# Performance work log

Hardware: AMD Instinct MI355X
Metric: run time of the kernel (lower is better)

Reference implementation:

```python
import jax, jax.numpy as jnp
import numpy as np

FEAT = 512
COND = 768
N_HEADS = 8
D_HEAD = 64
D_ATTN = N_HEADS * D_HEAD  # 512


def setup_inputs() -> dict:
    key = jax.random.key(0)
    ks = jax.random.split(key, 8)
    B, N, M = 16, 4096, 77
    x = jax.random.normal(ks[0], (B, N, FEAT), dtype=jnp.float32)
    cond = jax.random.normal(ks[1], (B, M, COND), dtype=jnp.float32)
    s_f = 1.0 / np.sqrt(FEAT)
    s_c = 1.0 / np.sqrt(COND)
    s_a = 1.0 / np.sqrt(D_ATTN)
    Wq = jax.random.normal(ks[2], (FEAT, D_ATTN), dtype=jnp.float32) * s_f
    Wk = jax.random.normal(ks[3], (COND, D_ATTN), dtype=jnp.float32) * s_c
    Wv = jax.random.normal(ks[4], (COND, D_ATTN), dtype=jnp.float32) * s_c
    Wo = jax.random.normal(ks[5], (D_ATTN, FEAT), dtype=jnp.float32) * s_a
    bo = jax.random.normal(ks[6], (FEAT,), dtype=jnp.float32) * 0.01
    return {"x": x, "cond": cond, "Wq": Wq, "Wk": Wk, "Wv": Wv, "Wo": Wo, "bo": bo}


def reference(x, cond, Wq, Wk, Wv, Wo, bo):
    B, N, _ = x.shape
    M = cond.shape[1]
    scale = D_HEAD ** (-0.5)
    # projections (no bias, as in nn.Linear(..., bias=False))
    q = (x @ Wq).reshape(B, N, N_HEADS, D_HEAD)
    k = (cond @ Wk).reshape(B, M, N_HEADS, D_HEAD)
    v = (cond @ Wv).reshape(B, M, N_HEADS, D_HEAD)
    attn = jnp.einsum('bihd,bjhd->bhij', q, k) * scale  # [B,H,N,M]
    attn = jax.nn.softmax(attn, axis=-1)  # split-half inplace softmax == plain softmax
    out = jnp.einsum('bhij,bjhd->bihd', attn, v).reshape(B, N, D_ATTN)
    return out @ Wo + bo
```

## Files before the change

### kernel.cpp

```cpp
#include <hip/hip_runtime.h>

typedef __attribute__((ext_vector_type(8))) _Float16 f16x8;
typedef __attribute__((ext_vector_type(4))) float f32x4;

#define B_SZ   16
#define N_SEQ  4096
#define M_CTX  77
#define M_PAD  96
#define NH     8

__device__ __forceinline__ _Float16 f2h(float x) { return (_Float16)x; }

__device__ __forceinline__ void gload16(const void* g, void* l) {
    __builtin_amdgcn_global_load_lds(
        (const __attribute__((address_space(1))) unsigned int*)g,
        (__attribute__((address_space(3))) unsigned int*)l, 16, 0, 0);
}

template<int C>
__device__ __forceinline__ float dppf(float x) {
    union { float f; int i; } u, v;
    u.f = x;
    v.i = __builtin_amdgcn_mov_dpp(u.i, C, 0xF, 0xF, true);
    return v.f;
}
__device__ __forceinline__ float rmax16(float x) {
    x = fmaxf(x, dppf<0xB1>(x));
    x = fmaxf(x, dppf<0x4E>(x));
    x = fmaxf(x, dppf<0x141>(x));
    x = fmaxf(x, dppf<0x140>(x));
    return x;
}
__device__ __forceinline__ float rsum16(float x) {
    x += dppf<0xB1>(x);
    x += dppf<0x4E>(x);
    x += dppf<0x141>(x);
    x += dppf<0x140>(x);
    return x;
}

__global__ __launch_bounds__(256)
void convert(const float4* __restrict__ x, f16x8* __restrict__ xh, int n8)
{
    int idx = blockIdx.x * 256 + threadIdx.x;
    int stride = gridDim.x * 256;
    for (int i = idx; i < n8; i += stride) {
        float4 a = x[2 * i];
        float4 b = x[2 * i + 1];
        f16x8 o;
        o[0] = f2h(a.x); o[1] = f2h(a.y); o[2] = f2h(a.z); o[3] = f2h(a.w);
        o[4] = f2h(b.x); o[5] = f2h(b.y); o[6] = f2h(b.z); o[7] = f2h(b.w);
        xh[i] = o;
    }
}

__global__ __launch_bounds__(256)
void prep(const float* __restrict__ Wq, const float* __restrict__ Wk,
          const float* __restrict__ Wv, const float* __restrict__ Wo,
          _Float16* __restrict__ WqT, _Float16* __restrict__ WkT,
          _Float16* __restrict__ WvT, _Float16* __restrict__ WoT)
{
    __shared__ float t[32][33];
    const float* W; _Float16* WT; int K; float scale = 1.0f;
    switch (blockIdx.z) {
        case 0:  W = Wq; WT = WqT; K = 512; scale = 0.125f; break;
        case 1:  W = Wk; WT = WkT; K = 768; break;
        case 2:  W = Wv; WT = WvT; K = 768; break;
        default: W = Wo; WT = WoT; K = 512; break;
    }
    const int ky = blockIdx.y;
    if (ky * 32 >= K) return;
    const int nx = blockIdx.x;
    const int tr = threadIdx.x >> 5, tc = threadIdx.x & 31;
#pragma unroll
    for (int i = 0; i < 4; ++i) {
        int kr = tr + i * 8;
        t[kr][tc] = W[(size_t)(ky * 32 + kr) * 512 + nx * 32 + tc];
    }
    __syncthreads();
#pragma unroll
    for (int i = 0; i < 4; ++i) {
        int nr = tr + i * 8;
        WT[(size_t)(nx * 32 + nr) * K + ky * 32 + tc] = f2h(t[tc][nr] * scale);
    }
}

__global__ __launch_bounds__(256)
void kv_proj(const float* __restrict__ cond, const _Float16* __restrict__ WkT,
             const _Float16* __restrict__ WvT, _Float16* __restrict__ Kswz,
             _Float16* __restrict__ Vswz)
{
    const int tid = threadIdx.x;
    const int l = tid & 63, w = tid >> 6;
    const int lrow = l & 15, lk = l >> 4;
    const int h = blockIdx.x, b = blockIdx.y, which = blockIdx.z;
    const _Float16* WT = which ? WvT : WkT;
    const float* cb = cond + (size_t)b * M_CTX * 768;

    f32x4 acc[5];
#pragma unroll
    for (int i = 0; i < 5; ++i)
#pragma unroll
        for (int e = 0; e < 4; ++e) acc[i][e] = 0.f;

    const int n = h * 64 + w * 16 + lrow;
    for (int kk = 0; kk < 24; ++kk) {
        f16x8 bfrag = *(const f16x8*)(WT + (size_t)n * 768 + kk * 32 + lk * 8);
#pragma unroll
        for (int rt = 0; rt < 5; ++rt) {
            int m = rt * 16 + lrow;
            f16x8 afrag;
#pragma unroll
            for (int j = 0; j < 8; ++j) afrag[j] = (_Float16)0.f;
            if (m < M_CTX) {
                const float* a = cb + (size_t)m * 768 + kk * 32 + lk * 8;
                float4 f0 = *(const float4*)a;
                float4 f1 = *(const float4*)(a + 4);
                afrag[0] = f2h(f0.x); afrag[1] = f2h(f0.y);
                afrag[2] = f2h(f0.z); afrag[3] = f2h(f0.w);
                afrag[4] = f2h(f1.x); afrag[5] = f2h(f1.y);
                afrag[6] = f2h(f1.z); afrag[7] = f2h(f1.w);
            }
            acc[rt] = __builtin_amdgcn_mfma_f32_16x16x32_f16(afrag, bfrag, acc[rt], 0, 0, 0);
        }
    }

    const int bh = b * NH + h;
    const int d = w * 16 + lrow;
    const int dhi = d >> 3, dlo = d & 7;
    if (which == 0) {
        _Float16* Kb = Kswz + (size_t)bh * (M_PAD * 64);
#pragma unroll
        for (int rt = 0; rt < 5; ++rt)
#pragma unroll
            for (int r = 0; r < 4; ++r) {
                int m = rt * 16 + lk * 4 + r;
                Kb[m * 64 + ((dhi ^ (m & 7)) * 8) + dlo] = f2h(acc[rt][r]);
            }
#pragma unroll
        for (int r = 0; r < 4; ++r) {
            int m = 80 + lk * 4 + r;
            Kb[m * 64 + ((dhi ^ (m & 7)) * 8) + dlo] = (_Float16)0.f;
        }
    } else {
        _Float16* Vb = Vswz + (size_t)bh * (64 * 128);
#pragma unroll
        for (int rt = 0; rt < 5; ++rt)
#pragma unroll
            for (int r = 0; r < 4; ++r) {
                int m = rt * 16 + lk * 4 + r;
                Vb[d * 128 + (((m >> 3) ^ dlo) * 8) + (m & 7)] = f2h(acc[rt][r]);
            }
#pragma unroll
        for (int r = 0; r < 4; ++r) {
            int m = 80 + lk * 4 + r;
            Vb[d * 128 + (((m >> 3) ^ dlo) * 8) + (m & 7)] = (_Float16)0.f;
        }
    }
}

template<int EMODE>
__global__ __launch_bounds__(256)
void gemm512(const _Float16* __restrict__ A, const _Float16* __restrict__ BT,
             void* __restrict__ Cv, const float* __restrict__ bias)
{
    __shared__ _Float16 As[128 * 64];
    __shared__ _Float16 Bs[128 * 64];

    const int bid = blockIdx.x;
    const int wg = (bid & 7) * 256 + (bid >> 3);
    const int rb = wg >> 2;
    const int cb = wg & 3;
    const size_t row0 = (size_t)rb * 128;
    const int col0 = cb * 128;

    const int tid = threadIdx.x;
    const int l = tid & 63;
    const int w = tid >> 6;
    const int wy = w >> 1, wx = w & 1;
    const int lrow = l & 15, lk = l >> 4;

    f32x4 acc[4][4];
#pragma unroll
    for (int i = 0; i < 4; ++i)
#pragma unroll
        for (int j = 0; j < 4; ++j)
#pragma unroll
            for (int e = 0; e < 4; ++e) acc[i][j][e] = 0.f;

    const int srow_in_seg = l >> 3;
    const int sslot = (l & 7) ^ (srow_in_seg & 7);
    const _Float16* a_src0 = A + (row0 + (size_t)(w * 32 + srow_in_seg)) * 512 + sslot * 8;
    const _Float16* b_src0 = BT + ((size_t)(col0 + w * 32 + srow_in_seg)) * 512 + sslot * 8;

    for (int kt = 0; kt < 8; ++kt) {
        const _Float16* ak = a_src0 + kt * 64;
        const _Float16* bk = b_src0 + kt * 64;
#pragma unroll
        for (int s = 0; s < 4; ++s) {
            gload16(ak + (size_t)s * 8 * 512, As + (w * 4 + s) * 512);
            gload16(bk + (size_t)s * 8 * 512, Bs + (w * 4 + s) * 512);
        }
        __syncthreads();

#pragma unroll
        for (int kk = 0; kk < 2; ++kk) {
            f16x8 af[4], bf[4];
#pragma unroll
            for (int mt = 0; mt < 4; ++mt) {
                int R = wy * 64 + mt * 16 + lrow;
                int p = (kk * 4 + lk) ^ (lrow & 7);
                af[mt] = *(const f16x8*)&As[R * 64 + p * 8];
            }
#pragma unroll
            for (int nt = 0; nt < 4; ++nt) {
                int R = wx * 64 + nt * 16 + lrow;
                int p = (kk * 4 + lk) ^ (lrow & 7);
                bf[nt] = *(const f16x8*)&Bs[R * 64 + p * 8];
            }
#pragma unroll
            for (int mt = 0; mt < 4; ++mt)
#pragma unroll
                for (int nt = 0; nt < 4; ++nt)
                    acc[mt][nt] = __builtin_amdgcn_mfma_f32_16x16x32_f16(af[mt], bf[nt], acc[mt][nt], 0, 0, 0);
        }
        __syncthreads();
    }

#pragma unroll
    for (int mt = 0; mt < 4; ++mt)
#pragma unroll
        for (int nt = 0; nt < 4; ++nt)
#pragma unroll
            for (int r = 0; r < 4; ++r) {
                size_t row = row0 + wy * 64 + mt * 16 + lk * 4 + r;
                int col = col0 + wx * 64 + nt * 16 + lrow;
                float v = acc[mt][nt][r];
                if (EMODE == 0) {
                    ((_Float16*)Cv)[row * 512 + col] = f2h(v);
                } else {
                    ((float*)Cv)[row * 512 + col] = v + bias[col];
                }
            }
}

__global__ __launch_bounds__(256)
void attn(const _Float16* __restrict__ Q, const _Float16* __restrict__ Kswz,
          const _Float16* __restrict__ Vswz, _Float16* __restrict__ AO)
{
    __shared__ _Float16 Ks[M_PAD * 64];
    __shared__ _Float16 Vs[64 * 128];
    __shared__ _Float16 Pl[4][16][104];

    const int tid = threadIdx.x;
    const int l = tid & 63, w = tid >> 6;
    const int lrow = l & 15, lk = l >> 4;
    const int chunk = blockIdx.x, h = blockIdx.y, b = blockIdx.z;
    const int bh = b * NH + h;

    {
        const _Float16* Kg = Kswz + (size_t)bh * (M_PAD * 64);
        const _Float16* Vg = Vswz + (size_t)bh * (64 * 128);
#pragma unroll
        for (int i = 0; i < 3; ++i) {
            int c = w * 3 + i;
            gload16(Kg + c * 512 + l * 8, Ks + c * 512);
        }
#pragma unroll
        for (int i = 0; i < 4; ++i) {
            int c = w * 4 + i;
            gload16(Vg + c * 512 + l * 8, Vs + c * 512);
        }
    }

    const size_t row0 = (size_t)b * N_SEQ + chunk * 256 + w * 64;
    f16x8 af[4][2];
    {
        const _Float16* Qb = Q + (row0 + lrow) * 512 + h * 64 + lk * 8;
#pragma unroll
        for (int mt = 0; mt < 4; ++mt)
#pragma unroll
            for (int kk = 0; kk < 2; ++kk)
                af[mt][kk] = *(const f16x8*)(Qb + (size_t)mt * 16 * 512 + kk * 32);
    }

    for (int idx = l; idx < 256; idx += 64)
        Pl[w][idx >> 4][80 + (idx & 15)] = (_Float16)0.f;

    __syncthreads();

    const bool m4ok = (lrow < 13);
    const int kswz = lrow & 7;

#pragma unroll
    for (int mt = 0; mt < 4; ++mt) {
        f32x4 s[5];
#pragma unroll
        for (int i = 0; i < 5; ++i)
#pragma unroll
            for (int e = 0; e < 4; ++e) s[i][e] = 0.f;
#pragma unroll
        for (int kk = 0; kk < 2; ++kk)
#pragma unroll
            for (int ct = 0; ct < 5; ++ct) {
                f16x8 kf = *(const f16x8*)&Ks[(ct * 16 + lrow) * 64 + (((kk * 4 + lk) ^ kswz) * 8)];
                s[ct] = __builtin_amdgcn_mfma_f32_16x16x32_f16(af[mt][kk], kf, s[ct], 0, 0, 0);
            }

        float rinv[4];
#pragma unroll
        for (int r = 0; r < 4; ++r) {
            float v0 = s[0][r], v1 = s[1][r], v2 = s[2][r], v3 = s[3][r], v4 = s[4][r];
            float mx = fmaxf(fmaxf(v0, v1), fmaxf(v2, v3));
            mx = fmaxf(mx, m4ok ? v4 : -1e30f);
            mx = rmax16(mx);
            float e0 = __expf(v0 - mx), e1 = __expf(v1 - mx);
            float e2 = __expf(v2 - mx), e3 = __expf(v3 - mx);
            float e4 = m4ok ? __expf(v4 - mx) : 0.f;
            float sum = ((e0 + e1) + (e2 + e3)) + e4;
            sum = rsum16(sum);
            rinv[r] = 1.0f / sum;
            int prow = lk * 4 + r;
            Pl[w][prow][lrow]      = f2h(e0);
            Pl[w][prow][16 + lrow] = f2h(e1);
            Pl[w][prow][32 + lrow] = f2h(e2);
            Pl[w][prow][48 + lrow] = f2h(e3);
            Pl[w][prow][64 + lrow] = f2h(e4);
        }

        f32x4 o[4];
#pragma unroll
        for (int i = 0; i < 4; ++i)
#pragma unroll
            for (int e2 = 0; e2 < 4; ++e2) o[i][e2] = 0.f;
#pragma unroll
        for (int kk = 0; kk < 3; ++kk) {
            f16x8 pa = *(const f16x8*)&Pl[w][lrow][kk * 32 + lk * 8];
#pragma unroll
            for (int ctd = 0; ctd < 4; ++ctd) {
                f16x8 vf = *(const f16x8*)&Vs[(ctd * 16 + lrow) * 128 + (((kk * 4 + lk) ^ kswz) * 8)];
                o[ctd] = __builtin_amdgcn_mfma_f32_16x16x32_f16(pa, vf, o[ctd], 0, 0, 0);
            }
        }

        const size_t rw = row0 + mt * 16 + lk * 4;
#pragma unroll
        for (int ctd = 0; ctd < 4; ++ctd)
#pragma unroll
            for (int r = 0; r < 4; ++r)
                AO[(rw + r) * 512 + h * 64 + ctd * 16 + lrow] = f2h(o[ctd][r] * rinv[r]);
    }
}

extern "C" void kernel_launch(void* const* d_in, const int* in_sizes, int n_in,
                              void* d_out, int out_size, void* d_ws, size_t ws_size,
                              hipStream_t stream)
{
    (void)in_sizes; (void)n_in; (void)out_size; (void)ws_size;
    const float* x    = (const float*)d_in[0];
    const float* cond = (const float*)d_in[1];
    const float* Wq   = (const float*)d_in[2];
    const float* Wk   = (const float*)d_in[3];
    const float* Wv   = (const float*)d_in[4];
    const float* Wo   = (const float*)d_in[5];
    const float* bo   = (const float*)d_in[6];

    char* ws = (char*)d_ws;
    _Float16* WqT  = (_Float16*)(ws);
    _Float16* WoT  = (_Float16*)(ws + 524288);
    _Float16* Kswz = (_Float16*)(ws + 1048576);
    _Float16* Vswz = (_Float16*)(ws + 2621440);
    _Float16* xh   = (_Float16*)(ws + 4718592);
    _Float16* WkT  = (_Float16*)(ws + 4718592);
    _Float16* WvT  = (_Float16*)(ws + 4718592 + 786432);
    _Float16* AO   = xh;
    _Float16* Qf   = (_Float16*)d_out;

    prep<<<dim3(16, 24, 4), 256, 0, stream>>>(Wq, Wk, Wv, Wo, WqT, WkT, WvT, WoT);
    kv_proj<<<dim3(8, 16, 2), 256, 0, stream>>>(cond, WkT, WvT, Kswz, Vswz);
    convert<<<dim3(2048), 256, 0, stream>>>((const float4*)x, (f16x8*)xh, 16 * 4096 * 512 / 8);
    gemm512<0><<<dim3(2048), 256, 0, stream>>>(xh, WqT, Qf, nullptr);
    attn<<<dim3(16, 8, 16), 256, 0, stream>>>(Qf, Kswz, Vswz, AO);
    gemm512<1><<<dim3(2048), 256, 0, stream>>>(AO, WoT, d_out, bo);
}
```

Measured before the change: 228.1 us.

## Rewrite projection GEMMs as 256x256 tiles with double-buffered async LDS pipeline

The Q and output projection GEMMs change from 128x128 tiles with 256 threads to 256x256 tiles with 512 threads and a 32-wide K step. LDS is double-buffered, and the global-to-LDS loads for the next A and B stages are issued between MFMA batches, synchronised with explicit vmcnt waits and raw barriers. MFMA sections are wrapped in raised wave priority. This targets fewer blocks, more operand reuse per tile and overlap of loads with compute, at the cost of 128KB of LDS, more registers, and a subtle hand-written wait/barrier schedule.

```diff
diff --git a/kernel.cpp b/kernel.cpp
--- a/kernel.cpp
+++ b/kernel.cpp
@@ -16,6 +16,10 @@
         (const __attribute__((address_space(1))) unsigned int*)g,
         (__attribute__((address_space(3))) unsigned int*)l, 16, 0, 0);
 }
+
+#define BAR()   asm volatile("s_barrier" ::: "memory")
+#define WAITV2() asm volatile("s_waitcnt vmcnt(2)" ::: "memory")
+#define WAITV0() asm volatile("s_waitcnt vmcnt(0)" ::: "memory")
 
 template<int C>
 __device__ __forceinline__ float dppf(float x) {
@@ -160,80 +164,98 @@
 }
 
 template<int EMODE>
-__global__ __launch_bounds__(256)
-void gemm512(const _Float16* __restrict__ A, const _Float16* __restrict__ BT,
+__global__ __launch_bounds__(512, 2)
+void gemm256(const _Float16* __restrict__ A, const _Float16* __restrict__ BT,
              void* __restrict__ Cv, const float* __restrict__ bias)
 {
-    __shared__ _Float16 As[128 * 64];
-    __shared__ _Float16 Bs[128 * 64];
+    __shared__ _Float16 As[32768];
+    __shared__ _Float16 Bs[32768];
 
     const int bid = blockIdx.x;
-    const int wg = (bid & 7) * 256 + (bid >> 3);
-    const int rb = wg >> 2;
-    const int cb = wg & 3;
-    const size_t row0 = (size_t)rb * 128;
-    const int col0 = cb * 128;
+    const int wg = (bid & 7) * 64 + (bid >> 3);
+    const int rb = wg >> 1, cb = wg & 1;
+    const size_t row0 = (size_t)rb * 256;
+    const int col0 = cb * 256;
 
     const int tid = threadIdx.x;
-    const int l = tid & 63;
-    const int w = tid >> 6;
-    const int wy = w >> 1, wx = w & 1;
+    const int l = tid & 63, w = tid >> 6;
+    const int wy = w >> 2, wx = w & 3;
     const int lrow = l & 15, lk = l >> 4;
 
-    f32x4 acc[4][4];
-#pragma unroll
-    for (int i = 0; i < 4; ++i)
+    f32x4 acc[8][4];
+#pragma unroll
+    for (int i = 0; i < 8; ++i)
 #pragma unroll
         for (int j = 0; j < 4; ++j)
 #pragma unroll
             for (int e = 0; e < 4; ++e) acc[i][j][e] = 0.f;
 
-    const int srow_in_seg = l >> 3;
-    const int sslot = (l & 7) ^ (srow_in_seg & 7);
-    const _Float16* a_src0 = A + (row0 + (size_t)(w * 32 + srow_in_seg)) * 512 + sslot * 8;
-    const _Float16* b_src0 = BT + ((size_t)(col0 + w * 32 + srow_in_seg)) * 512 + sslot * 8;
-
-    for (int kt = 0; kt < 8; ++kt) {
-        const _Float16* ak = a_src0 + kt * 64;
-        const _Float16* bk = b_src0 + kt * 64;
-#pragma unroll
-        for (int s = 0; s < 4; ++s) {
-            gload16(ak + (size_t)s * 8 * 512, As + (w * 4 + s) * 512);
-            gload16(bk + (size_t)s * 8 * 512, Bs + (w * 4 + s) * 512);
-        }
-        __syncthreads();
-
-#pragma unroll
-        for (int kk = 0; kk < 2; ++kk) {
-            f16x8 af[4], bf[4];
-#pragma unroll
-            for (int mt = 0; mt < 4; ++mt) {
-                int R = wy * 64 + mt * 16 + lrow;
-                int p = (kk * 4 + lk) ^ (lrow & 7);
-                af[mt] = *(const f16x8*)&As[R * 64 + p * 8];
-            }
-#pragma unroll
-            for (int nt = 0; nt < 4; ++nt) {
-                int R = wx * 64 + nt * 16 + lrow;
-                int p = (kk * 4 + lk) ^ (lrow & 7);
-                bf[nt] = *(const f16x8*)&Bs[R * 64 + p * 8];
-            }
-#pragma unroll
-            for (int mt = 0; mt < 4; ++mt)
-#pragma unroll
-                for (int nt = 0; nt < 4; ++nt)
-                    acc[mt][nt] = __builtin_amdgcn_mfma_f32_16x16x32_f16(af[mt], bf[nt], acc[mt][nt], 0, 0, 0);
-        }
-        __syncthreads();
-    }
-
-#pragma unroll
-    for (int mt = 0; mt < 4; ++mt)
+    const _Float16* a_src = A + (row0 + (size_t)(tid >> 2)) * 512 + (tid & 3) * 8;
+    const _Float16* b_src = BT + (size_t)(col0 + (tid >> 2)) * 512 + (tid & 3) * 8;
+    _Float16* As_d = &As[w * 512];
+    _Float16* Bs_d = &Bs[w * 512];
+
+    auto stageA = [&](int t) {
+        const _Float16* s = a_src + t * 32;
+        _Float16* d = As_d + (t & 1) * 8192;
+        gload16(s, d);
+        gload16(s + 128 * 512, d + 4096);
+    };
+    auto stageB = [&](int t) {
+        const _Float16* s = b_src + t * 32;
+        _Float16* d = Bs_d + (t & 1) * 8192;
+        gload16(s, d);
+        gload16(s + 128 * 512, d + 4096);
+    };
+
+    stageA(0); stageB(0); stageB(1);
+    WAITV2();
+    BAR();
+
+    const _Float16* Ar = &As[wy * 4096 + lrow * 32 + lk * 8];
+    const _Float16* Br = &Bs[(wx >> 1) * 4096 + ((wx & 1) * 64 + lrow) * 32 + lk * 8];
+
+    for (int t = 0; t < 16; ++t) {
+        const int bo = (t & 1) * 8192;
+        f16x8 af[4], bf[4];
+#pragma unroll
+        for (int i = 0; i < 4; ++i) af[i] = *(const f16x8*)(Ar + bo + i * 512);
+#pragma unroll
+        for (int i = 0; i < 4; ++i) bf[i] = *(const f16x8*)(Br + bo + i * 512);
+        if (t + 1 < 16) stageA(t + 1);
+        BAR();
+        __builtin_amdgcn_s_setprio(1);
+#pragma unroll
+        for (int mt = 0; mt < 4; ++mt)
+#pragma unroll
+            for (int nt = 0; nt < 4; ++nt)
+                acc[mt][nt] = __builtin_amdgcn_mfma_f32_16x16x32_f16(af[mt], bf[nt], acc[mt][nt], 0, 0, 0);
+        __builtin_amdgcn_s_setprio(0);
+
+        f16x8 ag[4];
+#pragma unroll
+        for (int i = 0; i < 4; ++i) ag[i] = *(const f16x8*)(Ar + bo + (4 + i) * 512);
+        if (t + 2 < 16) stageB(t + 2);
+        __builtin_amdgcn_s_setprio(1);
+#pragma unroll
+        for (int mt = 0; mt < 4; ++mt)
+#pragma unroll
+            for (int nt = 0; nt < 4; ++nt)
+                acc[4 + mt][nt] = __builtin_amdgcn_mfma_f32_16x16x32_f16(ag[mt], bf[nt], acc[4 + mt][nt], 0, 0, 0);
+        __builtin_amdgcn_s_setprio(0);
+
+        if (t <= 13)      WAITV2();
+        else if (t == 14) WAITV0();
+        if (t < 15) BAR();
+    }
+
+#pragma unroll
+    for (int mt = 0; mt < 8; ++mt)
 #pragma unroll
         for (int nt = 0; nt < 4; ++nt)
 #pragma unroll
             for (int r = 0; r < 4; ++r) {
-                size_t row = row0 + wy * 64 + mt * 16 + lk * 4 + r;
+                size_t row = row0 + wy * 128 + mt * 16 + lk * 4 + r;
                 int col = col0 + wx * 64 + nt * 16 + lrow;
                 float v = acc[mt][nt][r];
                 if (EMODE == 0) {
@@ -379,7 +401,7 @@
     prep<<<dim3(16, 24, 4), 256, 0, stream>>>(Wq, Wk, Wv, Wo, WqT, WkT, WvT, WoT);
     kv_proj<<<dim3(8, 16, 2), 256, 0, stream>>>(cond, WkT, WvT, Kswz, Vswz);
     convert<<<dim3(2048), 256, 0, stream>>>((const float4*)x, (f16x8*)xh, 16 * 4096 * 512 / 8);
-    gemm512<0><<<dim3(2048), 256, 0, stream>>>(xh, WqT, Qf, nullptr);
+    gemm256<0><<<dim3(512), 512, 0, stream>>>(xh, WqT, Qf, nullptr);
     attn<<<dim3(16, 8, 16), 256, 0, stream>>>(Qf, Kswz, Vswz, AO);
-    gemm512<1><<<dim3(2048), 256, 0, stream>>>(AO, WoT, d_out, bo);
-}
+    gemm256<1><<<dim3(512), 512, 0, stream>>>(AO, WoT, d_out, bo);
+}
```

Result: no change. 229.4 us (+0.6%).

## Fuse x conversion into Q GEMM and fuse attention with output projection

Applied to the files above, without the earlier changes.

The separate fp32-to-fp16 conversion kernel is removed. The Q projection now loads fp32 x tiles straight into LDS and converts them while building fragments. The attention kernel and the output-projection GEMM are merged: each 512-thread block handles 128 rows across all heads, stages the per-head attention output in a double-buffered LDS tile and accumulates the Wo product in registers, so the attention output never round-trips through global memory. In exchange, K and V are now read directly from global memory instead of LDS, the block holds a large register accumulator (which may lower occupancy), and the grid is smaller.

```diff
diff --git a/kernel.cpp b/kernel.cpp
--- a/kernel.cpp
+++ b/kernel.cpp
@@ -37,21 +37,6 @@
     x += dppf<0x141>(x);
     x += dppf<0x140>(x);
     return x;
-}
-
-__global__ __launch_bounds__(256)
-void convert(const float4* __restrict__ x, f16x8* __restrict__ xh, int n8)
-{
-    int idx = blockIdx.x * 256 + threadIdx.x;
-    int stride = gridDim.x * 256;
-    for (int i = idx; i < n8; i += stride) {
-        float4 a = x[2 * i];
-        float4 b = x[2 * i + 1];
-        f16x8 o;
-        o[0] = f2h(a.x); o[1] = f2h(a.y); o[2] = f2h(a.z); o[3] = f2h(a.w);
-        o[4] = f2h(b.x); o[5] = f2h(b.y); o[6] = f2h(b.z); o[7] = f2h(b.w);
-        xh[i] = o;
-    }
 }
 
 __global__ __launch_bounds__(256)
@@ -159,24 +144,21 @@
     }
 }
 
-template<int EMODE>
 __global__ __launch_bounds__(256)
-void gemm512(const _Float16* __restrict__ A, const _Float16* __restrict__ BT,
-             void* __restrict__ Cv, const float* __restrict__ bias)
-{
-    __shared__ _Float16 As[128 * 64];
+void gemm_q(const float* __restrict__ X, const _Float16* __restrict__ BT,
+            _Float16* __restrict__ C)
+{
+    __shared__ float    As[128 * 64];
     __shared__ _Float16 Bs[128 * 64];
 
     const int bid = blockIdx.x;
     const int wg = (bid & 7) * 256 + (bid >> 3);
-    const int rb = wg >> 2;
-    const int cb = wg & 3;
+    const int rb = wg >> 2, cb = wg & 3;
     const size_t row0 = (size_t)rb * 128;
     const int col0 = cb * 128;
 
     const int tid = threadIdx.x;
-    const int l = tid & 63;
-    const int w = tid >> 6;
+    const int l = tid & 63, w = tid >> 6;
     const int wy = w >> 1, wx = w & 1;
     const int lrow = l & 15, lk = l >> 4;
 
@@ -188,19 +170,24 @@
 #pragma unroll
             for (int e = 0; e < 4; ++e) acc[i][j][e] = 0.f;
 
-    const int srow_in_seg = l >> 3;
-    const int sslot = (l & 7) ^ (srow_in_seg & 7);
-    const _Float16* a_src0 = A + (row0 + (size_t)(w * 32 + srow_in_seg)) * 512 + sslot * 8;
-    const _Float16* b_src0 = BT + ((size_t)(col0 + w * 32 + srow_in_seg)) * 512 + sslot * 8;
+    const int r4 = l >> 4;
+    const int sA0 = (l & 15) ^ r4;
+    const int sA1 = (l & 15) ^ (4 + r4);
+    const float* xa0 = X + (row0 + w * 32 + r4) * 512 + sA0 * 4;
+    const float* xa1 = X + (row0 + w * 32 + r4) * 512 + sA1 * 4;
+    const int srow8 = l >> 3;
+    const int sB = (l & 7) ^ (srow8 & 7);
+    const _Float16* bsrc = BT + (size_t)(col0 + w * 32 + srow8) * 512 + sB * 8;
 
     for (int kt = 0; kt < 8; ++kt) {
-        const _Float16* ak = a_src0 + kt * 64;
-        const _Float16* bk = b_src0 + kt * 64;
-#pragma unroll
-        for (int s = 0; s < 4; ++s) {
-            gload16(ak + (size_t)s * 8 * 512, As + (w * 4 + s) * 512);
-            gload16(bk + (size_t)s * 8 * 512, Bs + (w * 4 + s) * 512);
-        }
+#pragma unroll
+        for (int i = 0; i < 8; ++i) {
+            const float* s = (i & 1 ? xa1 : xa0) + (size_t)i * 4 * 512 + kt * 64;
+            gload16(s, (char*)As + ((w * 8 + i) * 1024));
+        }
+#pragma unroll
+        for (int s4 = 0; s4 < 4; ++s4)
+            gload16(bsrc + (size_t)s4 * 8 * 512 + kt * 64, (char*)Bs + ((w * 4 + s4) * 1024));
         __syncthreads();
 
 #pragma unroll
@@ -208,9 +195,14 @@
             f16x8 af[4], bf[4];
 #pragma unroll
             for (int mt = 0; mt < 4; ++mt) {
-                int R = wy * 64 + mt * 16 + lrow;
-                int p = (kk * 4 + lk) ^ (lrow & 7);
-                af[mt] = *(const f16x8*)&As[R * 64 + p * 8];
+                int q = wy * 64 + mt * 16 + lrow;
+                int sb = kk * 8 + lk * 2, sw = lrow & 7;
+                f32x4 p0 = *(const f32x4*)&As[q * 64 + ((sb ^ sw) * 4)];
+                f32x4 p1 = *(const f32x4*)&As[q * 64 + (((sb + 1) ^ sw) * 4)];
+                f16x8 a;
+                a[0] = f2h(p0[0]); a[1] = f2h(p0[1]); a[2] = f2h(p0[2]); a[3] = f2h(p0[3]);
+                a[4] = f2h(p1[0]); a[5] = f2h(p1[1]); a[6] = f2h(p1[2]); a[7] = f2h(p1[3]);
+                af[mt] = a;
             }
 #pragma unroll
             for (int nt = 0; nt < 4; ++nt) {
@@ -235,77 +227,58 @@
             for (int r = 0; r < 4; ++r) {
                 size_t row = row0 + wy * 64 + mt * 16 + lk * 4 + r;
                 int col = col0 + wx * 64 + nt * 16 + lrow;
-                float v = acc[mt][nt][r];
-                if (EMODE == 0) {
-                    ((_Float16*)Cv)[row * 512 + col] = f2h(v);
-                } else {
-                    ((float*)Cv)[row * 512 + col] = v + bias[col];
-                }
-            }
-}
-
-__global__ __launch_bounds__(256)
-void attn(const _Float16* __restrict__ Q, const _Float16* __restrict__ Kswz,
-          const _Float16* __restrict__ Vswz, _Float16* __restrict__ AO)
-{
-    __shared__ _Float16 Ks[M_PAD * 64];
-    __shared__ _Float16 Vs[64 * 128];
-    __shared__ _Float16 Pl[4][16][104];
+                C[row * 512 + col] = f2h(acc[mt][nt][r]);
+            }
+}
+
+__global__ __launch_bounds__(512)
+void attn_oproj(const _Float16* __restrict__ Q, const _Float16* __restrict__ Kswz,
+                const _Float16* __restrict__ Vswz, const _Float16* __restrict__ WoT,
+                const float* __restrict__ bo, float* __restrict__ out)
+{
+    __shared__ _Float16 AO2[2][128 * 64];
+    __shared__ _Float16 Pl[8][16][104];
 
     const int tid = threadIdx.x;
     const int l = tid & 63, w = tid >> 6;
     const int lrow = l & 15, lk = l >> 4;
-    const int chunk = blockIdx.x, h = blockIdx.y, b = blockIdx.z;
-    const int bh = b * NH + h;
-
-    {
-        const _Float16* Kg = Kswz + (size_t)bh * (M_PAD * 64);
-        const _Float16* Vg = Vswz + (size_t)bh * (64 * 128);
-#pragma unroll
-        for (int i = 0; i < 3; ++i) {
-            int c = w * 3 + i;
-            gload16(Kg + c * 512 + l * 8, Ks + c * 512);
-        }
-#pragma unroll
-        for (int i = 0; i < 4; ++i) {
-            int c = w * 4 + i;
-            gload16(Vg + c * 512 + l * 8, Vs + c * 512);
-        }
-    }
-
-    const size_t row0 = (size_t)b * N_SEQ + chunk * 256 + w * 64;
-    f16x8 af[4][2];
-    {
-        const _Float16* Qb = Q + (row0 + lrow) * 512 + h * 64 + lk * 8;
-#pragma unroll
-        for (int mt = 0; mt < 4; ++mt)
-#pragma unroll
-            for (int kk = 0; kk < 2; ++kk)
-                af[mt][kk] = *(const f16x8*)(Qb + (size_t)mt * 16 * 512 + kk * 32);
-    }
+    const int chunk = blockIdx.x, b = blockIdx.y;
+    const size_t rowbase = (size_t)b * N_SEQ + chunk * 128;
+
+    f32x4 acc[8][4];
+#pragma unroll
+    for (int i = 0; i < 8; ++i)
+#pragma unroll
+        for (int j = 0; j < 4; ++j)
+#pragma unroll
+            for (int e = 0; e < 4; ++e) acc[i][j][e] = 0.f;
 
     for (int idx = l; idx < 256; idx += 64)
         Pl[w][idx >> 4][80 + (idx & 15)] = (_Float16)0.f;
 
-    __syncthreads();
-
     const bool m4ok = (lrow < 13);
-    const int kswz = lrow & 7;
-
-#pragma unroll
-    for (int mt = 0; mt < 4; ++mt) {
+
+    for (int h = 0; h < NH; ++h) {
+        const int bh = b * NH + h;
+
+        const _Float16* Qb = Q + (rowbase + w * 16 + lrow) * 512 + h * 64;
+        f16x8 qf0 = *(const f16x8*)(Qb + lk * 8);
+        f16x8 qf1 = *(const f16x8*)(Qb + 32 + lk * 8);
+
+        const _Float16* Kb = Kswz + (size_t)bh * (M_PAD * 64);
         f32x4 s[5];
 #pragma unroll
         for (int i = 0; i < 5; ++i)
 #pragma unroll
             for (int e = 0; e < 4; ++e) s[i][e] = 0.f;
 #pragma unroll
-        for (int kk = 0; kk < 2; ++kk)
-#pragma unroll
-            for (int ct = 0; ct < 5; ++ct) {
-                f16x8 kf = *(const f16x8*)&Ks[(ct * 16 + lrow) * 64 + (((kk * 4 + lk) ^ kswz) * 8)];
-                s[ct] = __builtin_amdgcn_mfma_f32_16x16x32_f16(af[mt][kk], kf, s[ct], 0, 0, 0);
-            }
+        for (int ct = 0; ct < 5; ++ct) {
+            int m = ct * 16 + lrow;
+            f16x8 k0 = *(const f16x8*)(Kb + m * 64 + ((lk ^ (m & 7)) * 8));
+            f16x8 k1 = *(const f16x8*)(Kb + m * 64 + (((4 + lk) ^ (m & 7)) * 8));
+            s[ct] = __builtin_amdgcn_mfma_f32_16x16x32_f16(qf0, k0, s[ct], 0, 0, 0);
+            s[ct] = __builtin_amdgcn_mfma_f32_16x16x32_f16(qf1, k1, s[ct], 0, 0, 0);
+        }
 
         float rinv[4];
 #pragma unroll
@@ -328,6 +301,7 @@
             Pl[w][prow][64 + lrow] = f2h(e4);
         }
 
+        const _Float16* Vb = Vswz + (size_t)bh * (64 * 128);
         f32x4 o[4];
 #pragma unroll
         for (int i = 0; i < 4; ++i)
@@ -338,18 +312,52 @@
             f16x8 pa = *(const f16x8*)&Pl[w][lrow][kk * 32 + lk * 8];
 #pragma unroll
             for (int ctd = 0; ctd < 4; ++ctd) {
-                f16x8 vf = *(const f16x8*)&Vs[(ctd * 16 + lrow) * 128 + (((kk * 4 + lk) ^ kswz) * 8)];
+                int d = ctd * 16 + lrow;
+                f16x8 vf = *(const f16x8*)(Vb + d * 128 + (((kk * 4 + lk) ^ (d & 7)) * 8));
                 o[ctd] = __builtin_amdgcn_mfma_f32_16x16x32_f16(pa, vf, o[ctd], 0, 0, 0);
             }
         }
 
-        const size_t rw = row0 + mt * 16 + lk * 4;
+        _Float16* A0 = AO2[h & 1];
 #pragma unroll
         for (int ctd = 0; ctd < 4; ++ctd)
 #pragma unroll
-            for (int r = 0; r < 4; ++r)
-                AO[(rw + r) * 512 + h * 64 + ctd * 16 + lrow] = f2h(o[ctd][r] * rinv[r]);
-    }
+            for (int r = 0; r < 4; ++r) {
+                int q = w * 16 + lk * 4 + r;
+                int col = ctd * 16 + lrow;
+                A0[q * 64 + (((col >> 3) ^ (q & 7)) * 8) + (col & 7)] =
+                    f2h(o[ctd][r] * rinv[r]);
+            }
+        __syncthreads();
+
+        const _Float16* Wb = WoT + h * 64;
+#pragma unroll
+        for (int kk = 0; kk < 2; ++kk) {
+            f16x8 bf[4];
+#pragma unroll
+            for (int nt = 0; nt < 4; ++nt)
+                bf[nt] = *(const f16x8*)(Wb + (size_t)(w * 64 + nt * 16 + lrow) * 512 + kk * 32 + lk * 8);
+#pragma unroll
+            for (int mt = 0; mt < 8; ++mt) {
+                int q = mt * 16 + lrow;
+                f16x8 a = *(const f16x8*)&A0[q * 64 + (((kk * 4 + lk) ^ (lrow & 7)) * 8)];
+#pragma unroll
+                for (int nt = 0; nt < 4; ++nt)
+                    acc[mt][nt] = __builtin_amdgcn_mfma_f32_16x16x32_f16(a, bf[nt], acc[mt][nt], 0, 0, 0);
+            }
+        }
+    }
+
+#pragma unroll
+    for (int mt = 0; mt < 8; ++mt)
+#pragma unroll
+        for (int nt = 0; nt < 4; ++nt)
+#pragma unroll
+            for (int r = 0; r < 4; ++r) {
+                size_t row = rowbase + mt * 16 + lk * 4 + r;
+                int col = w * 64 + nt * 16 + lrow;
+                out[row * 512 + col] = acc[mt][nt][r] + bo[col];
+            }
 }
 
 extern "C" void kernel_launch(void* const* d_in, const int* in_sizes, int n_in,
@@ -370,16 +378,12 @@
     _Float16* WoT  = (_Float16*)(ws + 524288);
     _Float16* Kswz = (_Float16*)(ws + 1048576);
     _Float16* Vswz = (_Float16*)(ws + 2621440);
-    _Float16* xh   = (_Float16*)(ws + 4718592);
+    _Float16* Qf   = (_Float16*)(ws + 4718592);
     _Float16* WkT  = (_Float16*)(ws + 4718592);
     _Float16* WvT  = (_Float16*)(ws + 4718592 + 786432);
-    _Float16* AO   = xh;
-    _Float16* Qf   = (_Float16*)d_out;
 
     prep<<<dim3(16, 24, 4), 256, 0, stream>>>(Wq, Wk, Wv, Wo, WqT, WkT, WvT, WoT);
     kv_proj<<<dim3(8, 16, 2), 256, 0, stream>>>(cond, WkT, WvT, Kswz, Vswz);
-    convert<<<dim3(2048), 256, 0, stream>>>((const float4*)x, (f16x8*)xh, 16 * 4096 * 512 / 8);
-    gemm512<0><<<dim3(2048), 256, 0, stream>>>(xh, WqT, Qf, nullptr);
-    attn<<<dim3(16, 8, 16), 256, 0, stream>>>(Qf, Kswz, Vswz, AO);
-    gemm512<1><<<dim3(2048), 256, 0, stream>>>(AO, WoT, d_out, bo);
-}
+    gemm_q<<<dim3(2048), 256, 0, stream>>>(x, WqT, Qf);
+    attn_oproj<<<dim3(32, 16), 512, 0, stream>>>(Qf, Kswz, Vswz, WoT, bo, (float*)d_out);
+}
```

Result: slower. 235.4 us (median of 4 runs) (+3.2%).

## Fuse fp32-to-fp16 conversion of x into Q projection GEMM with direct global loads

Applied to the files above, without the earlier changes.

Removes the separate convert kernel and reads fp32 x directly inside the Q projection GEMM, converting to fp16 in registers. The new Q GEMM also drops LDS staging and loads MFMA fragments straight from global memory in an unrolled loop. This avoids writing and re-reading a 64MB fp16 copy of x and one launch. The cost is that each wave loses LDS data sharing, so A and B tiles are fetched redundantly across waves and rely on the cache, with less coalesced access.

```diff
diff --git a/kernel.cpp b/kernel.cpp
--- a/kernel.cpp
+++ b/kernel.cpp
@@ -37,21 +37,6 @@
     x += dppf<0x141>(x);
     x += dppf<0x140>(x);
     return x;
-}
-
-__global__ __launch_bounds__(256)
-void convert(const float4* __restrict__ x, f16x8* __restrict__ xh, int n8)
-{
-    int idx = blockIdx.x * 256 + threadIdx.x;
-    int stride = gridDim.x * 256;
-    for (int i = idx; i < n8; i += stride) {
-        float4 a = x[2 * i];
-        float4 b = x[2 * i + 1];
-        f16x8 o;
-        o[0] = f2h(a.x); o[1] = f2h(a.y); o[2] = f2h(a.z); o[3] = f2h(a.w);
-        o[4] = f2h(b.x); o[5] = f2h(b.y); o[6] = f2h(b.z); o[7] = f2h(b.w);
-        xh[i] = o;
-    }
 }
 
 __global__ __launch_bounds__(256)
@@ -159,24 +144,18 @@
     }
 }
 
-template<int EMODE>
 __global__ __launch_bounds__(256)
-void gemm512(const _Float16* __restrict__ A, const _Float16* __restrict__ BT,
-             void* __restrict__ Cv, const float* __restrict__ bias)
-{
-    __shared__ _Float16 As[128 * 64];
-    __shared__ _Float16 Bs[128 * 64];
-
+void gemm_qd(const float* __restrict__ X, const _Float16* __restrict__ BT,
+             _Float16* __restrict__ C)
+{
     const int bid = blockIdx.x;
     const int wg = (bid & 7) * 256 + (bid >> 3);
-    const int rb = wg >> 2;
-    const int cb = wg & 3;
+    const int rb = wg >> 2, cb = wg & 3;
     const size_t row0 = (size_t)rb * 128;
     const int col0 = cb * 128;
 
     const int tid = threadIdx.x;
-    const int l = tid & 63;
-    const int w = tid >> 6;
+    const int l = tid & 63, w = tid >> 6;
     const int wy = w >> 1, wx = w & 1;
     const int lrow = l & 15, lk = l >> 4;
 
@@ -188,43 +167,30 @@
 #pragma unroll
             for (int e = 0; e < 4; ++e) acc[i][j][e] = 0.f;
 
-    const int srow_in_seg = l >> 3;
-    const int sslot = (l & 7) ^ (srow_in_seg & 7);
-    const _Float16* a_src0 = A + (row0 + (size_t)(w * 32 + srow_in_seg)) * 512 + sslot * 8;
-    const _Float16* b_src0 = BT + ((size_t)(col0 + w * 32 + srow_in_seg)) * 512 + sslot * 8;
-
-    for (int kt = 0; kt < 8; ++kt) {
-        const _Float16* ak = a_src0 + kt * 64;
-        const _Float16* bk = b_src0 + kt * 64;
-#pragma unroll
-        for (int s = 0; s < 4; ++s) {
-            gload16(ak + (size_t)s * 8 * 512, As + (w * 4 + s) * 512);
-            gload16(bk + (size_t)s * 8 * 512, Bs + (w * 4 + s) * 512);
-        }
-        __syncthreads();
-
-#pragma unroll
-        for (int kk = 0; kk < 2; ++kk) {
-            f16x8 af[4], bf[4];
-#pragma unroll
-            for (int mt = 0; mt < 4; ++mt) {
-                int R = wy * 64 + mt * 16 + lrow;
-                int p = (kk * 4 + lk) ^ (lrow & 7);
-                af[mt] = *(const f16x8*)&As[R * 64 + p * 8];
-            }
-#pragma unroll
-            for (int nt = 0; nt < 4; ++nt) {
-                int R = wx * 64 + nt * 16 + lrow;
-                int p = (kk * 4 + lk) ^ (lrow & 7);
-                bf[nt] = *(const f16x8*)&Bs[R * 64 + p * 8];
-            }
-#pragma unroll
-            for (int mt = 0; mt < 4; ++mt)
-#pragma unroll
-                for (int nt = 0; nt < 4; ++nt)
-                    acc[mt][nt] = __builtin_amdgcn_mfma_f32_16x16x32_f16(af[mt], bf[nt], acc[mt][nt], 0, 0, 0);
-        }
-        __syncthreads();
+    const float*    ab = X  + (row0 + wy * 64 + lrow) * 512 + lk * 8;
+    const _Float16* bb = BT + (size_t)(col0 + wx * 64 + lrow) * 512 + lk * 8;
+
+#pragma unroll 4
+    for (int kt = 0; kt < 16; ++kt) {
+        f16x8 af[4], bf[4];
+#pragma unroll
+        for (int mt = 0; mt < 4; ++mt) {
+            const float* a = ab + (size_t)mt * 16 * 512 + kt * 32;
+            float4 f0 = *(const float4*)a;
+            float4 f1 = *(const float4*)(a + 4);
+            f16x8 v;
+            v[0] = f2h(f0.x); v[1] = f2h(f0.y); v[2] = f2h(f0.z); v[3] = f2h(f0.w);
+            v[4] = f2h(f1.x); v[5] = f2h(f1.y); v[6] = f2h(f1.z); v[7] = f2h(f1.w);
+            af[mt] = v;
+        }
+#pragma unroll
+        for (int nt = 0; nt < 4; ++nt)
+            bf[nt] = *(const f16x8*)(bb + (size_t)nt * 16 * 512 + kt * 32);
+#pragma unroll
+        for (int mt = 0; mt < 4; ++mt)
+#pragma unroll
+            for (int nt = 0; nt < 4; ++nt)
+                acc[mt][nt] = __builtin_amdgcn_mfma_f32_16x16x32_f16(af[mt], bf[nt], acc[mt][nt], 0, 0, 0);
     }
 
 #pragma unroll
@@ -235,12 +201,7 @@
             for (int r = 0; r < 4; ++r) {
                 size_t row = row0 + wy * 64 + mt * 16 + lk * 4 + r;
                 int col = col0 + wx * 64 + nt * 16 + lrow;
-                float v = acc[mt][nt][r];
-                if (EMODE == 0) {
-                    ((_Float16*)Cv)[row * 512 + col] = f2h(v);
-                } else {
-                    ((float*)Cv)[row * 512 + col] = v + bias[col];
-                }
+                C[row * 512 + col] = f2h(acc[mt][nt][r]);
             }
 }
 
@@ -352,6 +313,85 @@
     }
 }
 
+__global__ __launch_bounds__(256)
+void gemm_o(const _Float16* __restrict__ A, const _Float16* __restrict__ BT,
+            float* __restrict__ Cv, const float* __restrict__ bias)
+{
+    __shared__ _Float16 As[128 * 64];
+    __shared__ _Float16 Bs[128 * 64];
+
+    const int bid = blockIdx.x;
+    const int wg = (bid & 7) * 256 + (bid >> 3);
+    const int rb = wg >> 2;
+    const int cb = wg & 3;
+    const size_t row0 = (size_t)rb * 128;
+    const int col0 = cb * 128;
+
+    const int tid = threadIdx.x;
+    const int l = tid & 63;
+    const int w = tid >> 6;
+    const int wy = w >> 1, wx = w & 1;
+    const int lrow = l & 15, lk = l >> 4;
+
+    f32x4 acc[4][4];
+#pragma unroll
+    for (int i = 0; i < 4; ++i)
+#pragma unroll
+        for (int j = 0; j < 4; ++j)
+#pragma unroll
+            for (int e = 0; e < 4; ++e) acc[i][j][e] = 0.f;
+
+    const int srow_in_seg = l >> 3;
+    const int sslot = (l & 7) ^ (srow_in_seg & 7);
+    const _Float16* a_src0 = A + (row0 + (size_t)(w * 32 + srow_in_seg)) * 512 + sslot * 8;
+    const _Float16* b_src0 = BT + ((size_t)(col0 + w * 32 + srow_in_seg)) * 512 + sslot * 8;
+
+    for (int kt = 0; kt < 8; ++kt) {
+        const _Float16* ak = a_src0 + kt * 64;
+        const _Float16* bk = b_src0 + kt * 64;
+#pragma unroll
+        for (int s = 0; s < 4; ++s) {
+            gload16(ak + (size_t)s * 8 * 512, As + (w * 4 + s) * 512);
+            gload16(bk + (size_t)s * 8 * 512, Bs + (w * 4 + s) * 512);
+        }
+        __syncthreads();
+
+#pragma unroll
+        for (int kk = 0; kk < 2; ++kk) {
+            f16x8 af[4], bf[4];
+#pragma unroll
+            for (int mt = 0; mt < 4; ++mt) {
+                int R = wy * 64 + mt * 16 + lrow;
+                int p = (kk * 4 + lk) ^ (lrow & 7);
+                af[mt] = *(const f16x8*)&As[R * 64 + p * 8];
+            }
+#pragma unroll
+            for (int nt = 0; nt < 4; ++nt) {
+                int R = wx * 64 + nt * 16 + lrow;
+                int p = (kk * 4 + lk) ^ (lrow & 7);
+                bf[nt] = *(const f16x8*)&Bs[R * 64 + p * 8];
+            }
+#pragma unroll
+            for (int mt = 0; mt < 4; ++mt)
+#pragma unroll
+                for (int nt = 0; nt < 4; ++nt)
+                    acc[mt][nt] = __builtin_amdgcn_mfma_f32_16x16x32_f16(af[mt], bf[nt], acc[mt][nt], 0, 0, 0);
+        }
+        __syncthreads();
+    }
+
+#pragma unroll
+    for (int mt = 0; mt < 4; ++mt)
+#pragma unroll
+        for (int nt = 0; nt < 4; ++nt)
+#pragma unroll
+            for (int r = 0; r < 4; ++r) {
+                size_t row = row0 + wy * 64 + mt * 16 + lk * 4 + r;
+                int col = col0 + wx * 64 + nt * 16 + lrow;
+                Cv[row * 512 + col] = acc[mt][nt][r] + bias[col];
+            }
+}
+
 extern "C" void kernel_launch(void* const* d_in, const int* in_sizes, int n_in,
                               void* d_out, int out_size, void* d_ws, size_t ws_size,
                               hipStream_t stream)
@@ -370,16 +410,14 @@
     _Float16* WoT  = (_Float16*)(ws + 524288);
     _Float16* Kswz = (_Float16*)(ws + 1048576);
     _Float16* Vswz = (_Float16*)(ws + 2621440);
-    _Float16* xh   = (_Float16*)(ws + 4718592);
+    _Float16* AO   = (_Float16*)(ws + 4718592);
     _Float16* WkT  = (_Float16*)(ws + 4718592);
     _Float16* WvT  = (_Float16*)(ws + 4718592 + 786432);
-    _Float16* AO   = xh;
     _Float16* Qf   = (_Float16*)d_out;
 
     prep<<<dim3(16, 24, 4), 256, 0, stream>>>(Wq, Wk, Wv, Wo, WqT, WkT, WvT, WoT);
     kv_proj<<<dim3(8, 16, 2), 256, 0, stream>>>(cond, WkT, WvT, Kswz, Vswz);
-    convert<<<dim3(2048), 256, 0, stream>>>((const float4*)x, (f16x8*)xh, 16 * 4096 * 512 / 8);
-    gemm512<0><<<dim3(2048), 256, 0, stream>>>(xh, WqT, Qf, nullptr);
+    gemm_qd<<<dim3(2048), 256, 0, stream>>>(x, WqT, Qf);
     attn<<<dim3(16, 8, 16), 256, 0, stream>>>(Qf, Kswz, Vswz, AO);
-    gemm512<1><<<dim3(2048), 256, 0, stream>>>(AO, WoT, d_out, bo);
-}
+    gemm_o<<<dim3(2048), 256, 0, stream>>>(AO, WoT, (float*)d_out, bo);
+}
```

Measured after the change: 327.3 us. 1.44x slower.
